# Optimization experiments

Measured on AMD Instinct MI355X. Metric: run time of the kernel, lower is better.

The kernel has to match this reference:

```python
import jax, jax.numpy as jnp
import numpy as np

N = 100000      # nodes
E = 3200000     # edges
F_IN = 128
HID = 64
NUM_CLASSES = 10
NUM_GRAPHS = 256


def setup_inputs() -> dict:
    key = jax.random.key(0)
    ks = jax.random.split(key, 12)
    x = jax.random.normal(ks[0], (N, F_IN), dtype=jnp.float32)
    edge_index = jax.random.randint(ks[1], (2, E), 0, N, dtype=jnp.int64)
    batch = jnp.sort(jax.random.randint(ks[2], (N,), 0, NUM_GRAPHS, dtype=jnp.int64))
    s = 1.0 / np.sqrt(F_IN)
    W1 = jax.random.uniform(ks[3], (F_IN, HID), jnp.float32, -s, s)
    b1 = jnp.zeros((HID,), jnp.float32)
    s2 = 1.0 / np.sqrt(HID)
    W2 = jax.random.uniform(ks[4], (HID, HID), jnp.float32, -s2, s2)
    b2 = jnp.zeros((HID,), jnp.float32)
    W3 = jax.random.uniform(ks[5], (HID, HID), jnp.float32, -s2, s2)
    b3 = jnp.zeros((HID,), jnp.float32)
    Wc = jax.random.uniform(ks[6], (HID, NUM_CLASSES), jnp.float32, -s2, s2)
    bc = jax.random.uniform(ks[7], (NUM_CLASSES,), jnp.float32, -s2, s2)
    return {"x": x, "edge_index": edge_index, "batch": batch,
            "W1": W1, "b1": b1, "W2": W2, "b2": b2, "W3": W3, "b3": b3,
            "Wc": Wc, "bc": bc}


def _gcn_norm(edge_index, num_nodes):
    # add self-loops, compute symmetric normalization D^-1/2 A_hat D^-1/2
    loop = jnp.arange(num_nodes, dtype=edge_index.dtype)
    src = jnp.concatenate([edge_index[0], loop])
    dst = jnp.concatenate([edge_index[1], loop])
    deg = jax.ops.segment_sum(jnp.ones_like(dst, dtype=jnp.float32), dst,
                              num_segments=num_nodes)
    dinv = jax.lax.rsqrt(deg)  # deg >= 1 due to self-loops
    norm = dinv[src] * dinv[dst]  # [E+N]
    return src, dst, norm


def _gcn_layer(x, W, b, src, dst, norm, num_nodes):
    h = x @ W                              # [N, H] dense transform first (PyG order)
    msg = norm[:, None] * h[src]           # gather + scale
    agg = jax.ops.segment_sum(msg, dst, num_segments=num_nodes)  # scatter-add
    return agg + b


def reference(x, edge_index, batch, W1, b1, W2, b2, W3, b3, Wc, bc):
    num_nodes = x.shape[0]
    src, dst, norm = _gcn_norm(edge_index, num_nodes)
    h = jax.nn.relu(_gcn_layer(x, W1, b1, src, dst, norm, num_nodes))
    h = jax.nn.relu(_gcn_layer(h, W2, b2, src, dst, norm, num_nodes))
    h = jax.nn.relu(_gcn_layer(h, W3, b3, src, dst, norm, num_nodes))
    # global mean pool over graphs
    sums = jax.ops.segment_sum(h, batch, num_segments=NUM_GRAPHS)
    cnt = jax.ops.segment_sum(jnp.ones((num_nodes,), jnp.float32), batch,
                              num_segments=NUM_GRAPHS)
    pooled = sums / jnp.maximum(cnt, 1.0)[:, None]   # [G, HID]
    return pooled @ Wc + bc                          # [G, NUM_CLASSES]
```

## Files before the change

kernel.cpp:

```cpp
#include <hip/hip_runtime.h>


#define NSUB 512
#define MAXNODES 256

typedef __attribute__((ext_vector_type(8))) short bf16x8;
typedef __attribute__((ext_vector_type(4))) float f32x4;

__device__ __forceinline__ unsigned short f2bf(float x) {
  unsigned u = __float_as_uint(x);
  u += 0x7FFFu + ((u >> 16) & 1u);
  return (unsigned short)(u >> 16);
}
__device__ __forceinline__ float bf2f(unsigned short h) {
  return __uint_as_float((unsigned)h << 16);
}
__device__ __forceinline__ float uf(unsigned u) { return __uint_as_float(u); }

__device__ __forceinline__ int idx32(const int* p, long long i, bool wide) {
  return __builtin_nontemporal_load(p + (wide ? 2 * i : i));
}

__global__ __launch_bounds__(1024) void k_part(const void* __restrict__ eiv, int E,
                                               int* __restrict__ flag, int cap2,
                                               int* __restrict__ scur,
                                               unsigned* __restrict__ ebuf2, int N) {
  __shared__ int cnt[NSUB];
  __shared__ int base[NSUB];
  __shared__ int off[NSUB];
  __shared__ int s_any;
  const unsigned* eu = (const unsigned*)eiv;
  const int* ei = (const int*)eiv;
  const int tid = threadIdx.x;
  if (tid == 0) s_any = 0;
  __syncthreads();
  unsigned vv = 0;
  for (int i = tid; i < 8192; i += 1024) vv |= eu[2 * i + 1];
  if (vv) atomicOr(&s_any, 1);
  for (int i = tid; i < NSUB; i += 1024) { cnt[i] = 0; off[i] = 0; }
  __syncthreads();
  const bool wide = (s_any == 0);
  if (blockIdx.x == 0 && tid == 0) *flag = wide ? 1 : 0;
  const int chunk = (E + gridDim.x - 1) / gridDim.x;
  const int c0 = blockIdx.x * chunk;
  const int c1 = (c0 + chunk < E) ? c0 + chunk : E;
  for (int e = c0 + tid; e < c1; e += 1024) {
    const int d = idx32(ei, (long long)E + e, wide);
    const int b = (int)(((long long)d * NSUB) / N);
    atomicAdd(&cnt[b], 1);
  }
  __syncthreads();
  for (int i = tid; i < NSUB; i += 1024) base[i] = atomicAdd(&scur[i], cnt[i]);
  __syncthreads();
  const long long cap = (long long)NSUB * cap2;
  for (int e = c0 + tid; e < c1; e += 1024) {
    const int d = idx32(ei, (long long)E + e, wide);
    const int s = idx32(ei, e, wide);
    const int b = (int)(((long long)d * NSUB) / N);
    const int nlo = (int)(((long long)N * b + NSUB - 1) / NSUB);
    const int o = atomicAdd(&off[b], 1);
    long long pos = (long long)b * cap2 + base[b] + o;
    if (pos >= cap) pos = cap - 1;
    ebuf2[pos] = ((unsigned)(d - nlo) << 24) | (unsigned)s;
  }
}

#define STASHJ 16
__global__ __launch_bounds__(512) void k_build(const unsigned* __restrict__ ebuf2,
                                               const int* __restrict__ scur, int cap2,
                                               int* __restrict__ rowptr,
                                               float* __restrict__ dinv,
                                               int* __restrict__ csr, int N) {
  __shared__ int sc[NSUB];
  __shared__ int hist[256];
  __shared__ int pref[256];
  const int s = blockIdx.x;
  const int t = threadIdx.x;
  if (t < NSUB) sc[t] = scur[t];
  __syncthreads();
  for (int off = 1; off < NSUB; off <<= 1) {
    int tv = 0;
    if (t < NSUB && t >= off) tv = sc[t - off];
    __syncthreads();
    if (t < NSUB) sc[t] += tv;
    __syncthreads();
  }
  const int mycnt = scur[s];
  const int sb = sc[s] - mycnt;
  const int total = sc[NSUB - 1];
  int nlo = (int)(((long long)N * s + NSUB - 1) / NSUB);
  int nhi = (int)(((long long)N * (s + 1) + NSUB - 1) / NSUB);
  if (nhi > N) nhi = N;
  const int nn = nhi - nlo;
  if (t < 256) hist[t] = 0;
  __syncthreads();
  const long long e0 = (long long)s * cap2;
  const long long e1 = e0 + mycnt;
  unsigned stash[STASHJ];
#pragma unroll
  for (int j = 0; j < STASHJ; ++j) {
    const long long e = e0 + t + (long long)j * 512;
    if (e < e1) {
      const unsigned v = __builtin_nontemporal_load(&ebuf2[e]);
      stash[j] = v;
      atomicAdd(&hist[v >> 24], 1);
    }
  }
  for (long long e = e0 + t + (long long)STASHJ * 512; e < e1; e += 512) {
    const unsigned v = __builtin_nontemporal_load(&ebuf2[e]);
    atomicAdd(&hist[v >> 24], 1);
  }
  __syncthreads();
  int h = 0;
  if (t < 256) {
    h = hist[t];
    pref[t] = h;
  }
  __syncthreads();
  for (int off = 1; off < 256; off <<= 1) {
    int tv = 0;
    if (t < 256 && t >= off) tv = pref[t - off];
    __syncthreads();
    if (t < 256) pref[t] += tv;
    __syncthreads();
  }
  if (t < 256) {
    const int cur0 = sb + pref[t] - h;
    if (t < nn) {
      rowptr[nlo + t] = cur0;
      dinv[nlo + t] = rsqrtf((float)(h + 1));
    }
    hist[t] = cur0;
  }
  if (s == NSUB - 1 && t == 0) rowptr[N] = total;
  __syncthreads();
#pragma unroll
  for (int j = 0; j < STASHJ; ++j) {
    const long long e = e0 + t + (long long)j * 512;
    if (e < e1) {
      const unsigned v = stash[j];
      const int pos = atomicAdd(&hist[v >> 24], 1);
      csr[pos] = (int)(v & 0x00FFFFFFu);
    }
  }
  for (long long e = e0 + t + (long long)STASHJ * 512; e < e1; e += 512) {
    const unsigned v = ebuf2[e];
    const int pos = atomicAdd(&hist[v >> 24], 1);
    csr[pos] = (int)(v & 0x00FFFFFFu);
  }
}

template <int K, bool BF16IN>
__global__ __launch_bounds__(256) void k_gemm_mfma(const void* __restrict__ Xv,
                                                   const float* __restrict__ Wg,
                                                   const float* __restrict__ dinv,
                                                   unsigned short* __restrict__ HS,
                                                   int N) {
  __shared__ short Xl[64 * K];
  __shared__ short Wt[64 * K];
  const int t = threadIdx.x;
  const long long r0 = (long long)blockIdx.x * 64;
  const int rows = (int)((N - r0) < 64 ? (N - r0) : 64);

  for (int idx = t; idx < K * 64; idx += 256) {
    const int k = idx >> 6, n = idx & 63;
    Wt[n * K + (((k >> 3) ^ (n & 7)) << 3) + (k & 7)] = (short)f2bf(Wg[idx]);
  }
  const int CH = K / 8;
#pragma unroll
  for (int p = 0; p < K / 32; ++p) {
    const int c = p * 256 + t;
    const int row = c / CH, ch = c % CH;
    const int src = (row < rows) ? row : 0;
    bf16x8 h;
    if constexpr (BF16IN) {
      h = *(const bf16x8*)&((const unsigned short*)Xv)[(r0 + src) * K + ch * 8];
    } else {
      const float* X = (const float*)Xv;
      const float4 v0 = *(const float4*)&X[(r0 + src) * K + ch * 8];
      const float4 v1 = *(const float4*)&X[(r0 + src) * K + ch * 8 + 4];
      h[0] = (short)f2bf(v0.x); h[1] = (short)f2bf(v0.y);
      h[2] = (short)f2bf(v0.z); h[3] = (short)f2bf(v0.w);
      h[4] = (short)f2bf(v1.x); h[5] = (short)f2bf(v1.y);
      h[6] = (short)f2bf(v1.z); h[7] = (short)f2bf(v1.w);
    }
    *(bf16x8*)&Xl[row * K + ((ch ^ (row & 7)) << 3)] = h;
  }
  __syncthreads();

  const int lane = t & 63, w = t >> 6;
  const int lo = lane & 15, hi = lane >> 4;
  const int rowa = w * 16 + lo;

  f32x4 acc[4];
#pragma unroll
  for (int i = 0; i < 4; ++i) acc[i] = (f32x4){0.f, 0.f, 0.f, 0.f};

  bf16x8 a[K / 32];
#pragma unroll
  for (int kk = 0; kk < K / 32; ++kk)
    a[kk] = *(const bf16x8*)&Xl[rowa * K + (((kk * 4 + hi) ^ (rowa & 7)) << 3)];

#pragma unroll
  for (int n0 = 0; n0 < 4; ++n0) {
    const int n = n0 * 16 + lo;
#pragma unroll
    for (int kk = 0; kk < K / 32; ++kk) {
      const bf16x8 b = *(const bf16x8*)&Wt[n * K + (((kk * 4 + hi) ^ (n & 7)) << 3)];
      acc[n0] = __builtin_amdgcn_mfma_f32_16x16x32_bf16(a[kk], b, acc[n0], 0, 0, 0);
    }
  }

  float dv[4];
#pragma unroll
  for (int r = 0; r < 4; ++r) {
    const int rr = w * 16 + hi * 4 + r;
    dv[r] = dinv[r0 + (rr < rows ? rr : 0)];
  }
#pragma unroll
  for (int n0 = 0; n0 < 4; ++n0) {
#pragma unroll
    for (int r = 0; r < 4; ++r) {
      const int rr = w * 16 + hi * 4 + r;
      if (rr < rows)
        HS[(r0 + rr) * 64 + n0 * 16 + lo] = f2bf(dv[r] * acc[n0][r]);
    }
  }
}

__global__ __launch_bounds__(256) void k_agg_gemm(
    const unsigned short* __restrict__ HSin, const int* __restrict__ rowptr,
    const int* __restrict__ csr, const float* __restrict__ dinv,
    const float* __restrict__ bias, const float* __restrict__ Wg,
    unsigned short* __restrict__ HSout, int N) {
  __shared__ short Xl[64 * 64];
  __shared__ short Wt[64 * 64];
  const int t = threadIdx.x;
  const long long r0 = (long long)blockIdx.x * 64;
  const int rows = (int)((N - r0) < 64 ? (N - r0) : 64);
  for (int idx = t; idx < 64 * 64; idx += 256) {
    const int k = idx >> 6, n = idx & 63;
    Wt[n * 64 + (((k >> 3) ^ (n & 7)) << 3) + (k & 7)] = (short)f2bf(Wg[idx]);
  }
  if (rows < 64) {
    for (int i = t; i < 64 * 64; i += 256) Xl[i] = 0;
  }
  __syncthreads();

  const int lane = t & 63;
  const int wid = t >> 6;
  const int c4 = lane & 15;
  const int q = lane >> 4;
  const float bb0 = bias[4 * c4 + 0], bb1 = bias[4 * c4 + 1];
  const float bb2 = bias[4 * c4 + 2], bb3 = bias[4 * c4 + 3];
  const uint2* __restrict__ H8 = (const uint2*)HSin;
  const unsigned M = 0xffff0000u;
  for (int i = 0; i < 16; ++i) {
    const int row = wid * 16 + i;
    if (row >= rows) break;
    const int node = (int)(r0 + row);
    const int s0 = rowptr[node], s1 = rowptr[node + 1];
    float a0 = 0.f, a1 = 0.f, a2 = 0.f, a3 = 0.f;
    float c0 = 0.f, c1 = 0.f, c2 = 0.f, c3 = 0.f;
    if (q == 0) {
      const uint2 u = H8[(long long)node * 16 + c4];
      a0 += uf(u.x << 16); a1 += uf(u.x & M);
      a2 += uf(u.y << 16); a3 += uf(u.y & M);
    }
    for (int base = s0; base < s1; base += 64) {
      int m = s1 - base;
      if (m > 64) m = 64;
      const int idx = (base + lane < s1) ? csr[base + lane] : 0;
      const int ng = m >> 2;
      int g = 0;
      for (; g + 2 <= ng; g += 2) {
        const int e0 = __shfl(idx, 4 * g + q, 64);
        const int e1 = __shfl(idx, 4 * g + 4 + q, 64);
        const uint2 u0 = H8[(long long)e0 * 16 + c4];
        const uint2 u1 = H8[(long long)e1 * 16 + c4];
        a0 += uf(u0.x << 16); a1 += uf(u0.x & M);
        a2 += uf(u0.y << 16); a3 += uf(u0.y & M);
        c0 += uf(u1.x << 16); c1 += uf(u1.x & M);
        c2 += uf(u1.y << 16); c3 += uf(u1.y & M);
      }
      for (; g < ng; ++g) {
        const int e0 = __shfl(idx, 4 * g + q, 64);
        const uint2 u0 = H8[(long long)e0 * 16 + c4];
        a0 += uf(u0.x << 16); a1 += uf(u0.x & M);
        a2 += uf(u0.y << 16); a3 += uf(u0.y & M);
      }
      const int rm = m & 3;
      if (rm) {
        const int e = __shfl(idx, (m & ~3) + (q < rm ? q : 0), 64);
        if (q < rm) {
          const uint2 u = H8[(long long)e * 16 + c4];
          a0 += uf(u.x << 16); a1 += uf(u.x & M);
          a2 += uf(u.y << 16); a3 += uf(u.y & M);
        }
      }
    }
    a0 += c0; a1 += c1; a2 += c2; a3 += c3;
    a0 += __shfl_xor(a0, 16, 64); a0 += __shfl_xor(a0, 32, 64);
    a1 += __shfl_xor(a1, 16, 64); a1 += __shfl_xor(a1, 32, 64);
    a2 += __shfl_xor(a2, 16, 64); a2 += __shfl_xor(a2, 32, 64);
    a3 += __shfl_xor(a3, 16, 64); a3 += __shfl_xor(a3, 32, 64);
    if (q == 0) {
      const float dv = dinv[node];
      const unsigned short o0 = f2bf(fmaxf(fmaf(dv, a0, bb0), 0.f));
      const unsigned short o1 = f2bf(fmaxf(fmaf(dv, a1, bb1), 0.f));
      const unsigned short o2 = f2bf(fmaxf(fmaf(dv, a2, bb2), 0.f));
      const unsigned short o3 = f2bf(fmaxf(fmaf(dv, a3, bb3), 0.f));
      uint2 o;
      o.x = (unsigned)o0 | ((unsigned)o1 << 16);
      o.y = (unsigned)o2 | ((unsigned)o3 << 16);
      const int ch = c4 >> 1;
      *(uint2*)&Xl[row * 64 + ((ch ^ (row & 7)) << 3) + (c4 & 1) * 4] = o;
    }
  }
  __syncthreads();

  const int lo = lane & 15, hi = lane >> 4;
  const int rowa = wid * 16 + lo;
  f32x4 acc[4];
#pragma unroll
  for (int i = 0; i < 4; ++i) acc[i] = (f32x4){0.f, 0.f, 0.f, 0.f};
  bf16x8 a[2];
#pragma unroll
  for (int kk = 0; kk < 2; ++kk)
    a[kk] = *(const bf16x8*)&Xl[rowa * 64 + (((kk * 4 + hi) ^ (rowa & 7)) << 3)];
#pragma unroll
  for (int n0 = 0; n0 < 4; ++n0) {
    const int n = n0 * 16 + lo;
#pragma unroll
    for (int kk = 0; kk < 2; ++kk) {
      const bf16x8 b = *(const bf16x8*)&Wt[n * 64 + (((kk * 4 + hi) ^ (n & 7)) << 3)];
      acc[n0] = __builtin_amdgcn_mfma_f32_16x16x32_bf16(a[kk], b, acc[n0], 0, 0, 0);
    }
  }
  float dvv[4];
#pragma unroll
  for (int r = 0; r < 4; ++r) {
    const int rr = wid * 16 + hi * 4 + r;
    dvv[r] = dinv[r0 + (rr < rows ? rr : 0)];
  }
#pragma unroll
  for (int n0 = 0; n0 < 4; ++n0) {
#pragma unroll
    for (int r = 0; r < 4; ++r) {
      const int rr = wid * 16 + hi * 4 + r;
      if (rr < rows)
        HSout[(r0 + rr) * 64 + n0 * 16 + lo] = f2bf(dvv[r] * acc[n0][r]);
    }
  }
}

__global__ __launch_bounds__(256) void k_agg_pool(
    const unsigned short* __restrict__ HS, const int* __restrict__ rowptr,
    const int* __restrict__ csr, const float* __restrict__ dinv,
    const float* __restrict__ bias, const void* __restrict__ batch,
    const int* __restrict__ flag, float* __restrict__ pooled, int N) {
  const int t = threadIdx.x;
  const long long r0 = (long long)blockIdx.x * 64;
  const int rows = (int)((N - r0) < 64 ? (N - r0) : 64);
  const int lane = t & 63;
  const int wid = t >> 6;
  const int c4 = lane & 15;
  const int q = lane >> 4;
  const bool wideB = (*flag != 0);
  const int* bi = (const int*)batch;
  const float bb0 = bias[4 * c4 + 0], bb1 = bias[4 * c4 + 1];
  const float bb2 = bias[4 * c4 + 2], bb3 = bias[4 * c4 + 3];
  const uint2* __restrict__ H8 = (const uint2*)HS;
  const unsigned M = 0xffff0000u;
  float ps0 = 0.f, ps1 = 0.f, ps2 = 0.f, ps3 = 0.f;
  int gcur = -1;
  for (int i = 0; i < 16; ++i) {
    const int row = wid * 16 + i;
    if (row >= rows) break;
    const int node = (int)(r0 + row);
    const int g = wideB ? (int)((const long long*)batch)[node] : bi[node];
    const int s0 = rowptr[node], s1 = rowptr[node + 1];
    float a0 = 0.f, a1 = 0.f, a2 = 0.f, a3 = 0.f;
    float c0 = 0.f, c1 = 0.f, c2 = 0.f, c3 = 0.f;
    if (q == 0) {
      const uint2 u = H8[(long long)node * 16 + c4];
      a0 += uf(u.x << 16); a1 += uf(u.x & M);
      a2 += uf(u.y << 16); a3 += uf(u.y & M);
    }
    for (int base = s0; base < s1; base += 64) {
      int m = s1 - base;
      if (m > 64) m = 64;
      const int idx = (base + lane < s1) ? csr[base + lane] : 0;
      const int ng = m >> 2;
      int gg = 0;
      for (; gg + 2 <= ng; gg += 2) {
        const int e0 = __shfl(idx, 4 * gg + q, 64);
        const int e1 = __shfl(idx, 4 * gg + 4 + q, 64);
        const uint2 u0 = H8[(long long)e0 * 16 + c4];
        const uint2 u1 = H8[(long long)e1 * 16 + c4];
        a0 += uf(u0.x << 16); a1 += uf(u0.x & M);
        a2 += uf(u0.y << 16); a3 += uf(u0.y & M);
        c0 += uf(u1.x << 16); c1 += uf(u1.x & M);
        c2 += uf(u1.y << 16); c3 += uf(u1.y & M);
      }
      for (; gg < ng; ++gg) {
        const int e0 = __shfl(idx, 4 * gg + q, 64);
        const uint2 u0 = H8[(long long)e0 * 16 + c4];
        a0 += uf(u0.x << 16); a1 += uf(u0.x & M);
        a2 += uf(u0.y << 16); a3 += uf(u0.y & M);
      }
      const int rm = m & 3;
      if (rm) {
        const int e = __shfl(idx, (m & ~3) + (q < rm ? q : 0), 64);
        if (q < rm) {
          const uint2 u = H8[(long long)e * 16 + c4];
          a0 += uf(u.x << 16); a1 += uf(u.x & M);
          a2 += uf(u.y << 16); a3 += uf(u.y & M);
        }
      }
    }
    a0 += c0; a1 += c1; a2 += c2; a3 += c3;
    a0 += __shfl_xor(a0, 16, 64); a0 += __shfl_xor(a0, 32, 64);
    a1 += __shfl_xor(a1, 16, 64); a1 += __shfl_xor(a1, 32, 64);
    a2 += __shfl_xor(a2, 16, 64); a2 += __shfl_xor(a2, 32, 64);
    a3 += __shfl_xor(a3, 16, 64); a3 += __shfl_xor(a3, 32, 64);
    if (g != gcur) {
      if (gcur >= 0 && q == 0) {
        atomicAdd(&pooled[gcur * 64 + 4 * c4 + 0], ps0);
        atomicAdd(&pooled[gcur * 64 + 4 * c4 + 1], ps1);
        atomicAdd(&pooled[gcur * 64 + 4 * c4 + 2], ps2);
        atomicAdd(&pooled[gcur * 64 + 4 * c4 + 3], ps3);
      }
      ps0 = ps1 = ps2 = ps3 = 0.f;
      gcur = g;
    }
    if (q == 0) {
      const float dv = dinv[node];
      ps0 += fmaxf(fmaf(dv, a0, bb0), 0.f);
      ps1 += fmaxf(fmaf(dv, a1, bb1), 0.f);
      ps2 += fmaxf(fmaf(dv, a2, bb2), 0.f);
      ps3 += fmaxf(fmaf(dv, a3, bb3), 0.f);
    }
  }
  if (gcur >= 0 && q == 0) {
    atomicAdd(&pooled[gcur * 64 + 4 * c4 + 0], ps0);
    atomicAdd(&pooled[gcur * 64 + 4 * c4 + 1], ps1);
    atomicAdd(&pooled[gcur * 64 + 4 * c4 + 2], ps2);
    atomicAdd(&pooled[gcur * 64 + 4 * c4 + 3], ps3);
  }
}

__global__ __launch_bounds__(64) void k_cls(const float* __restrict__ pooled,
                                            const void* __restrict__ batch,
                                            const int* __restrict__ flag,
                                            const float* __restrict__ Wc,
                                            const float* __restrict__ bc,
                                            float* __restrict__ out, int N) {
  __shared__ int se[2];
  __shared__ float pl[64];
  const bool wide = (*flag != 0);
  const int g = blockIdx.x;
  if (threadIdx.x < 2) {
    int target = g + threadIdx.x;
    int lo = 0, hi = N;
    while (lo < hi) {
      int mid = (lo + hi) >> 1;
      long long v = wide ? ((const long long*)batch)[mid] : (long long)((const int*)batch)[mid];
      if (v < target) lo = mid + 1; else hi = mid;
    }
    se[threadIdx.x] = lo;
  }
  __syncthreads();
  const float cnt = (float)(se[1] - se[0]);
  pl[threadIdx.x] = pooled[g * 64 + threadIdx.x] / fmaxf(cnt, 1.f);
  __syncthreads();
  if (threadIdx.x < 10) {
    float a = bc[threadIdx.x];
#pragma unroll
    for (int h = 0; h < 64; ++h) a += pl[h] * Wc[h * 10 + threadIdx.x];
    out[g * 10 + threadIdx.x] = a;
  }
}

extern "C" void kernel_launch(void* const* d_in, const int* in_sizes, int n_in,
                              void* d_out, int out_size, void* d_ws, size_t ws_size,
                              hipStream_t stream) {
  const float* x = (const float*)d_in[0];
  const void* ei = d_in[1];
  const void* batch = d_in[2];
  const float* W1 = (const float*)d_in[3];
  const float* b1 = (const float*)d_in[4];
  const float* W2 = (const float*)d_in[5];
  const float* b2 = (const float*)d_in[6];
  const float* W3 = (const float*)d_in[7];
  const float* b3 = (const float*)d_in[8];
  const float* Wc = (const float*)d_in[9];
  const float* bc = (const float*)d_in[10];
  float* out = (float*)d_out;

  const int N = in_sizes[0] / 128;
  const int E = in_sizes[1] / 2;
  const int G = out_size / 10;
  const int cap2 = E / NSUB + E / NSUB / 8 + 64;

  char* W = (char*)d_ws;
  size_t off = 0;
  auto take = [&](size_t b) -> void* {
    void* p = W + off;
    off += (b + 255) & ~(size_t)255;
    return p;
  };
  int* flag = (int*)take(4);
  int* rowptr = (int*)take((size_t)4 * (N + 1));
  int* scur = (int*)take((size_t)4 * NSUB);
  float* pooled = (float*)take((size_t)4 * G * 64);
  float* dinv = (float*)take((size_t)4 * N);
  int* csr = (int*)take((size_t)4 * E);
  unsigned short* hsA = (unsigned short*)take((size_t)2 * N * 64);
  unsigned short* hsB = (unsigned short*)take((size_t)2 * N * 64);
  unsigned* ebuf2 = (unsigned*)take((size_t)4 * NSUB * cap2);
  (void)ws_size;

  hipMemsetAsync(scur, 0, (size_t)2048 + (size_t)4 * G * 64, stream);

  k_part<<<512, 1024, 0, stream>>>(ei, E, flag, cap2, scur, ebuf2, N);
  k_build<<<NSUB, 512, 0, stream>>>(ebuf2, scur, cap2, rowptr, dinv, csr, N);

  const int TILES = (N + 63) / 64;
  k_gemm_mfma<128, false><<<TILES, 256, 0, stream>>>(x, W1, dinv, hsA, N);
  k_agg_gemm<<<TILES, 256, 0, stream>>>(hsA, rowptr, csr, dinv, b1, W2, hsB, N);
  k_agg_gemm<<<TILES, 256, 0, stream>>>(hsB, rowptr, csr, dinv, b2, W3, hsA, N);
  k_agg_pool<<<TILES, 256, 0, stream>>>(hsA, rowptr, csr, dinv, b3, batch, flag,
                                        pooled, N);
  k_cls<<<G, 64, 0, stream>>>(pooled, batch, flag, Wc, bc, out, N);
}
```

Baseline: 309.1 us.

## Stash partition edges in registers and use 512-thread aggregation blocks

The partition kernel now keeps the first PSTASH chunks of packed edges and their bucket ids in registers, so the scatter pass does not reread those indices from global memory. The aggregation kernels go from 256 to 512 threads per 64-row tile. Each wave now aggregates 8 rows instead of 16, and the MFMA epilogue is split so each wave computes 2 of the 4 column blocks. This is meant to cut repeated edge-index loads and give more waves per tile to hide gather latency, at the cost of extra register pressure and a larger block size.

```diff
diff --git a/kernel.cpp b/kernel.cpp
--- a/kernel.cpp
+++ b/kernel.cpp
@@ -3,6 +3,7 @@
 
 #define NSUB 512
 #define MAXNODES 256
+#define PSTASH 8
 
 typedef __attribute__((ext_vector_type(8))) short bf16x8;
 typedef __attribute__((ext_vector_type(4))) float f32x4;
@@ -44,7 +45,23 @@
   const int chunk = (E + gridDim.x - 1) / gridDim.x;
   const int c0 = blockIdx.x * chunk;
   const int c1 = (c0 + chunk < E) ? c0 + chunk : E;
-  for (int e = c0 + tid; e < c1; e += 1024) {
+  unsigned pk[PSTASH];
+  int pb[PSTASH];
+#pragma unroll
+  for (int j = 0; j < PSTASH; ++j) {
+    pb[j] = -1;
+    const int e = c0 + j * 1024 + tid;
+    if (e < c1) {
+      const int d = idx32(ei, (long long)E + e, wide);
+      const int s = idx32(ei, e, wide);
+      const int b = (int)(((long long)d * NSUB) / N);
+      const int nlo = (int)(((long long)N * b + NSUB - 1) / NSUB);
+      pk[j] = ((unsigned)(d - nlo) << 24) | (unsigned)s;
+      pb[j] = b;
+      atomicAdd(&cnt[b], 1);
+    }
+  }
+  for (int e = c0 + PSTASH * 1024 + tid; e < c1; e += 1024) {
     const int d = idx32(ei, (long long)E + e, wide);
     const int b = (int)(((long long)d * NSUB) / N);
     atomicAdd(&cnt[b], 1);
@@ -53,7 +70,17 @@
   for (int i = tid; i < NSUB; i += 1024) base[i] = atomicAdd(&scur[i], cnt[i]);
   __syncthreads();
   const long long cap = (long long)NSUB * cap2;
-  for (int e = c0 + tid; e < c1; e += 1024) {
+#pragma unroll
+  for (int j = 0; j < PSTASH; ++j) {
+    if (pb[j] >= 0) {
+      const int b = pb[j];
+      const int o = atomicAdd(&off[b], 1);
+      long long pos = (long long)b * cap2 + base[b] + o;
+      if (pos >= cap) pos = cap - 1;
+      ebuf2[pos] = pk[j];
+    }
+  }
+  for (int e = c0 + PSTASH * 1024 + tid; e < c1; e += 1024) {
     const int d = idx32(ei, (long long)E + e, wide);
     const int s = idx32(ei, e, wide);
     const int b = (int)(((long long)d * NSUB) / N);
@@ -228,7 +255,7 @@
   }
 }
 
-__global__ __launch_bounds__(256) void k_agg_gemm(
+__global__ __launch_bounds__(512) void k_agg_gemm(
     const unsigned short* __restrict__ HSin, const int* __restrict__ rowptr,
     const int* __restrict__ csr, const float* __restrict__ dinv,
     const float* __restrict__ bias, const float* __restrict__ Wg,
@@ -238,12 +265,12 @@
   const int t = threadIdx.x;
   const long long r0 = (long long)blockIdx.x * 64;
   const int rows = (int)((N - r0) < 64 ? (N - r0) : 64);
-  for (int idx = t; idx < 64 * 64; idx += 256) {
+  for (int idx = t; idx < 64 * 64; idx += 512) {
     const int k = idx >> 6, n = idx & 63;
     Wt[n * 64 + (((k >> 3) ^ (n & 7)) << 3) + (k & 7)] = (short)f2bf(Wg[idx]);
   }
   if (rows < 64) {
-    for (int i = t; i < 64 * 64; i += 256) Xl[i] = 0;
+    for (int i = t; i < 64 * 64; i += 512) Xl[i] = 0;
   }
   __syncthreads();
 
@@ -255,8 +282,8 @@
   const float bb2 = bias[4 * c4 + 2], bb3 = bias[4 * c4 + 3];
   const uint2* __restrict__ H8 = (const uint2*)HSin;
   const unsigned M = 0xffff0000u;
-  for (int i = 0; i < 16; ++i) {
-    const int row = wid * 16 + i;
+  for (int i = 0; i < 8; ++i) {
+    const int row = wid * 8 + i;
     if (row >= rows) break;
     const int node = (int)(r0 + row);
     const int s0 = rowptr[node], s1 = rowptr[node + 1];
@@ -320,41 +347,43 @@
   __syncthreads();
 
   const int lo = lane & 15, hi = lane >> 4;
-  const int rowa = wid * 16 + lo;
-  f32x4 acc[4];
-#pragma unroll
-  for (int i = 0; i < 4; ++i) acc[i] = (f32x4){0.f, 0.f, 0.f, 0.f};
+  const int wrow = (wid & 3) * 16;
+  const int wcol = (wid >> 2) * 2;
+  const int rowa = wrow + lo;
+  f32x4 acc[2];
+#pragma unroll
+  for (int i = 0; i < 2; ++i) acc[i] = (f32x4){0.f, 0.f, 0.f, 0.f};
   bf16x8 a[2];
 #pragma unroll
   for (int kk = 0; kk < 2; ++kk)
     a[kk] = *(const bf16x8*)&Xl[rowa * 64 + (((kk * 4 + hi) ^ (rowa & 7)) << 3)];
 #pragma unroll
-  for (int n0 = 0; n0 < 4; ++n0) {
-    const int n = n0 * 16 + lo;
+  for (int p = 0; p < 2; ++p) {
+    const int n = (wcol + p) * 16 + lo;
 #pragma unroll
     for (int kk = 0; kk < 2; ++kk) {
       const bf16x8 b = *(const bf16x8*)&Wt[n * 64 + (((kk * 4 + hi) ^ (n & 7)) << 3)];
-      acc[n0] = __builtin_amdgcn_mfma_f32_16x16x32_bf16(a[kk], b, acc[n0], 0, 0, 0);
+      acc[p] = __builtin_amdgcn_mfma_f32_16x16x32_bf16(a[kk], b, acc[p], 0, 0, 0);
     }
   }
   float dvv[4];
 #pragma unroll
   for (int r = 0; r < 4; ++r) {
-    const int rr = wid * 16 + hi * 4 + r;
+    const int rr = wrow + hi * 4 + r;
     dvv[r] = dinv[r0 + (rr < rows ? rr : 0)];
   }
 #pragma unroll
-  for (int n0 = 0; n0 < 4; ++n0) {
+  for (int p = 0; p < 2; ++p) {
 #pragma unroll
     for (int r = 0; r < 4; ++r) {
-      const int rr = wid * 16 + hi * 4 + r;
+      const int rr = wrow + hi * 4 + r;
       if (rr < rows)
-        HSout[(r0 + rr) * 64 + n0 * 16 + lo] = f2bf(dvv[r] * acc[n0][r]);
-    }
-  }
-}
-
-__global__ __launch_bounds__(256) void k_agg_pool(
+        HSout[(r0 + rr) * 64 + (wcol + p) * 16 + lo] = f2bf(dvv[r] * acc[p][r]);
+    }
+  }
+}
+
+__global__ __launch_bounds__(512) void k_agg_pool(
     const unsigned short* __restrict__ HS, const int* __restrict__ rowptr,
     const int* __restrict__ csr, const float* __restrict__ dinv,
     const float* __restrict__ bias, const void* __restrict__ batch,
@@ -374,8 +403,8 @@
   const unsigned M = 0xffff0000u;
   float ps0 = 0.f, ps1 = 0.f, ps2 = 0.f, ps3 = 0.f;
   int gcur = -1;
-  for (int i = 0; i < 16; ++i) {
-    const int row = wid * 16 + i;
+  for (int i = 0; i < 8; ++i) {
+    const int row = wid * 8 + i;
     if (row >= rows) break;
     const int node = (int)(r0 + row);
     const int g = wideB ? (int)((const long long*)batch)[node] : bi[node];
@@ -528,9 +557,9 @@
 
   const int TILES = (N + 63) / 64;
   k_gemm_mfma<128, false><<<TILES, 256, 0, stream>>>(x, W1, dinv, hsA, N);
-  k_agg_gemm<<<TILES, 256, 0, stream>>>(hsA, rowptr, csr, dinv, b1, W2, hsB, N);
-  k_agg_gemm<<<TILES, 256, 0, stream>>>(hsB, rowptr, csr, dinv, b2, W3, hsA, N);
-  k_agg_pool<<<TILES, 256, 0, stream>>>(hsA, rowptr, csr, dinv, b3, batch, flag,
+  k_agg_gemm<<<TILES, 512, 0, stream>>>(hsA, rowptr, csr, dinv, b1, W2, hsB, N);
+  k_agg_gemm<<<TILES, 512, 0, stream>>>(hsB, rowptr, csr, dinv, b2, W3, hsA, N);
+  k_agg_pool<<<TILES, 512, 0, stream>>>(hsA, rowptr, csr, dinv, b3, batch, flag,
                                         pooled, N);
   k_cls<<<G, 64, 0, stream>>>(pooled, batch, flag, Wc, bc, out, N);
 }
```

Measured after the change: 293.0 us. -5.2%, faster.
